# Kernel optimization log

Measured on AMD Instinct MI355X. Metric: run time of the kernel, lower is better.

## Reference

```python
import jax, jax.numpy as jnp
import numpy as np

S, B, E, D, A = 4096, 16, 1024, 1024, 512


def setup_inputs() -> dict:
    key = jax.random.key(0)
    ks = jax.random.split(key, 8)
    inv = lambda n: 1.0 / np.sqrt(n)
    return {
        "encoder_padded_last_layer_states": jax.random.normal(ks[0], (S, B, E), jnp.float32),
        "decoder_previous_time_step_state": jax.random.normal(ks[1], (1, B, D), jnp.float32),
        "We": jax.random.uniform(ks[2], (E, A), jnp.float32, -inv(E), inv(E)),
        "be": jax.random.uniform(ks[3], (A,), jnp.float32, -inv(E), inv(E)),
        "Wd": jax.random.uniform(ks[4], (D, A), jnp.float32, -inv(D), inv(D)),
        "bd": jax.random.uniform(ks[5], (A,), jnp.float32, -inv(D), inv(D)),
        "Ws": jax.random.uniform(ks[6], (A, 1), jnp.float32, -inv(A), inv(A)),
        "bs": jax.random.uniform(ks[7], (1,), jnp.float32, -inv(A), inv(A)),
    }


def reference(encoder_padded_last_layer_states, decoder_previous_time_step_state,
              We, be, Wd, bd, Ws, bs):
    enc = encoder_padded_last_layer_states  # [S, B, E]
    dec = decoder_previous_time_step_state  # [1, B, D]
    weighted_e = enc @ We + be              # [S, B, A]
    weighted_d = dec @ Wd + bd              # [1, B, A] broadcasts over S
    scores = jnp.tanh(weighted_e + weighted_d) @ Ws + bs  # [S, B, 1]
    alpha = jax.nn.softmax(scores, axis=0)  # softmax over time dim
    # alpha^T [B,1,S] bmm enc^T [B,S,E] -> [B,1,E] -> squeeze -> [B,E]
    contexts = jnp.einsum("sbo,sbe->be", alpha, enc)
    return contexts
```

## Files before the change

kernel.cpp:

```cpp
#include <hip/hip_runtime.h>
#include <hip/hip_bf16.h>

#define S_DIM 4096
#define B_DIM 16
#define E_DIM 1024
#define D_DIM 1024
#define A_DIM 512
#define M_DIM (S_DIM * B_DIM)
#define BK 64
#define NKS (E_DIM / BK)
#define MT 64

typedef __bf16 bf16x8 __attribute__((ext_vector_type(8)));
typedef float f32x4 __attribute__((ext_vector_type(4)));
typedef unsigned short u16;

__device__ __forceinline__ u16 f2bf(float f) {
    unsigned u = __builtin_bit_cast(unsigned, f);
    u += 0x7fffu + ((u >> 16) & 1u);
    return (u16)(u >> 16);
}
__device__ __forceinline__ unsigned pack2(float a, float b) {
    return (unsigned)f2bf(a) | ((unsigned)f2bf(b) << 16);
}

__device__ __forceinline__ void gload_lds16(const void* g, void* l) {
    __builtin_amdgcn_global_load_lds(
        (const __attribute__((address_space(1))) unsigned*)g,
        (__attribute__((address_space(3))) unsigned*)l, 16, 0, 0);
}

__global__ void k_prep_we(const float* __restrict__ We, u16* __restrict__ WeT) {
    const int gid = blockIdx.x * 256 + threadIdx.x;
    const int ks = gid >> 12, rem = gid & 4095;
    const int a = rem >> 3, d = rem & 7;
    const int c = d ^ (a & 7);
    const int e0 = ks * BK + c * 8;
    float v[8];
#pragma unroll
    for (int i = 0; i < 8; ++i) v[i] = We[(size_t)(e0 + i) * A_DIM + a];
    uint4 h;
    h.x = pack2(v[0], v[1]); h.y = pack2(v[2], v[3]);
    h.z = pack2(v[4], v[5]); h.w = pack2(v[6], v[7]);
    *reinterpret_cast<uint4*>(WeT + (size_t)ks * A_DIM * BK + a * BK + d * 8) = h;
}

__global__ void k_comb(const float* __restrict__ dec, const float* __restrict__ Wd,
                       const float* __restrict__ bd, const float* __restrict__ be,
                       float* __restrict__ comb) {
    __shared__ float red[4][64];
    const int a0 = blockIdx.x * 64;
    const int b = blockIdx.y;
    const int t = threadIdx.x;
    const int al = t & 63, w = t >> 6;
    float acc = 0.f;
    const float* dp = dec + (size_t)b * D_DIM + w * 256;
    const float* wp = Wd + (size_t)w * 256 * A_DIM + a0 + al;
    for (int d = 0; d < 256; ++d)
        acc += dp[d] * wp[(size_t)d * A_DIM];
    red[w][al] = acc;
    __syncthreads();
    if (t < 64)
        comb[b * A_DIM + a0 + t] =
            red[0][t] + red[1][t] + red[2][t] + red[3][t] + bd[a0 + t] + be[a0 + t];
}

__global__ __launch_bounds__(256, 2)
void k_scores(const float* __restrict__ enc, const u16* __restrict__ WeT,
              const float* __restrict__ comb, const float* __restrict__ Wsv,
              float* __restrict__ scores) {
    __shared__ __align__(16) u16 As[MT * BK];
    __shared__ __align__(16) u16 Bs[A_DIM * BK];

    const int tid = threadIdx.x;
    const int lane = tid & 63;
    const int wc = tid >> 6;
    const int l15 = lane & 15, lhi = lane >> 4;
    const int blockRow = blockIdx.x * MT;

    f32x4 acc[4][8];
#pragma unroll
    for (int mf = 0; mf < 4; ++mf)
#pragma unroll
        for (int nf = 0; nf < 8; ++nf)
            acc[mf][nf] = f32x4{0.f, 0.f, 0.f, 0.f};

    const int bOff = wc * 16384 + lane * 16;

    for (int ks = 0; ks < NKS; ++ks) {
        const int k0 = ks * BK;
        const char* gsrc = (const char*)WeT + (size_t)ks * A_DIM * BK * 2 + bOff;
        char* ldst = (char*)Bs + bOff;
#pragma unroll
        for (int i = 0; i < 16; ++i)
            gload_lds16(gsrc + i * 1024, ldst + i * 1024);
#pragma unroll
        for (int h = 0; h < 2; ++h) {
            const int g = tid + h * 256;
            const int r = g >> 3, d = g & 7;
            const int c = d ^ (r & 7);
            const float* src = enc + (size_t)(blockRow + r) * E_DIM + k0 + c * 8;
            const float4 v0 = *reinterpret_cast<const float4*>(src);
            const float4 v1 = *reinterpret_cast<const float4*>(src + 4);
            uint4 hh;
            hh.x = pack2(v0.x, v0.y); hh.y = pack2(v0.z, v0.w);
            hh.z = pack2(v1.x, v1.y); hh.w = pack2(v1.z, v1.w);
            *reinterpret_cast<uint4*>((char*)As + r * 128 + d * 16) = hh;
        }
        __syncthreads();
#pragma unroll
        for (int kk = 0; kk < 2; ++kk) {
            bf16x8 af[4];
#pragma unroll
            for (int mf = 0; mf < 4; ++mf) {
                const int rr = mf * 16 + l15;
                af[mf] = *reinterpret_cast<const bf16x8*>(
                    (const char*)As + rr * 128 + ((kk * 64 + lhi * 16) ^ ((rr & 7) << 4)));
            }
#pragma unroll
            for (int nf = 0; nf < 8; ++nf) {
                const int br = wc * 128 + nf * 16 + l15;
                const bf16x8 bfv = *reinterpret_cast<const bf16x8*>(
                    (const char*)Bs + br * 128 + ((kk * 64 + lhi * 16) ^ ((br & 7) << 4)));
#pragma unroll
                for (int mf = 0; mf < 4; ++mf)
                    acc[mf][nf] = __builtin_amdgcn_mfma_f32_16x16x32_bf16(
                        af[mf], bfv, acc[mf][nf], 0, 0, 0);
            }
        }
        __syncthreads();
    }

    float* combLDS = reinterpret_cast<float*>(Bs);
    float* sred = reinterpret_cast<float*>(As);
#pragma unroll
    for (int i = 0; i < 8; ++i) {
        const int idx = tid + i * 256;
        reinterpret_cast<float4*>(combLDS)[idx] = reinterpret_cast<const float4*>(comb)[idx];
    }
    if (tid < MT) sred[tid] = 0.f;
    __syncthreads();

    float part[4][4] = {};
#pragma unroll
    for (int nf = 0; nf < 8; ++nf) {
        const int C = wc * 128 + nf * 16 + l15;
        const float wsv = Wsv[C];
#pragma unroll
        for (int mf = 0; mf < 4; ++mf) {
#pragma unroll
            for (int j = 0; j < 4; ++j) {
                const int Rl = mf * 16 + lhi * 4 + j;
                const int b = (blockRow + Rl) & (B_DIM - 1);
                const float x = acc[mf][nf][j] + combLDS[b * A_DIM + C];
                const float e = __expf(-2.f * fabsf(x));
                float th = (1.f - e) / (1.f + e);
                th = (x < 0.f) ? -th : th;
                part[mf][j] += th * wsv;
            }
        }
    }
#pragma unroll
    for (int off = 1; off < 16; off <<= 1)
#pragma unroll
        for (int mf = 0; mf < 4; ++mf)
#pragma unroll
            for (int j = 0; j < 4; ++j)
                part[mf][j] += __shfl_xor(part[mf][j], off, 64);
    if (l15 == 0) {
#pragma unroll
        for (int mf = 0; mf < 4; ++mf)
#pragma unroll
            for (int j = 0; j < 4; ++j)
                atomicAdd(&sred[mf * 16 + lhi * 4 + j], part[mf][j]);
    }
    __syncthreads();
    if (tid < MT) {
        const int rr = blockRow + tid;
        scores[(size_t)(rr & (B_DIM - 1)) * S_DIM + (rr >> 4)] = sred[tid];
    }
}

__global__ void k_softmax(const float* __restrict__ scores, float* __restrict__ alpha) {
    __shared__ float red[8];
    const int b = blockIdx.x;
    const int tid = threadIdx.x;
    const float* sc = scores + (size_t)b * S_DIM;
    float m = -1e30f;
    for (int i = tid; i < S_DIM; i += 256) m = fmaxf(m, sc[i]);
#pragma unroll
    for (int off = 32; off; off >>= 1) m = fmaxf(m, __shfl_xor(m, off, 64));
    if ((tid & 63) == 0) red[tid >> 6] = m;
    __syncthreads();
    m = fmaxf(fmaxf(red[0], red[1]), fmaxf(red[2], red[3]));
    float s = 0.f;
    for (int i = tid; i < S_DIM; i += 256) s += __expf(sc[i] - m);
#pragma unroll
    for (int off = 32; off; off >>= 1) s += __shfl_xor(s, off, 64);
    if ((tid & 63) == 0) red[4 + (tid >> 6)] = s;
    __syncthreads();
    const float inv = 1.f / (red[4] + red[5] + red[6] + red[7]);
    float* al = alpha + (size_t)b * S_DIM;
    for (int i = tid; i < S_DIM; i += 256) al[i] = __expf(sc[i] - m) * inv;
}

__global__ void k_ctx1(const float* __restrict__ enc, const float* __restrict__ alpha,
                       float* __restrict__ partial) {
    const int b = blockIdx.y, ch = blockIdx.x, tid = threadIdx.x;
    const int s0 = ch * 64;
    float4 av = make_float4(0.f, 0.f, 0.f, 0.f);
    const float* al = alpha + (size_t)b * S_DIM + s0;
    for (int s = 0; s < 64; ++s) {
        const float a = al[s];
        const float4 v = *reinterpret_cast<const float4*>(
            enc + ((size_t)(s0 + s) * B_DIM + b) * E_DIM + tid * 4);
        av.x += a * v.x; av.y += a * v.y; av.z += a * v.z; av.w += a * v.w;
    }
    reinterpret_cast<float4*>(partial)[((size_t)b * 64 + ch) * 256 + tid] = av;
}

__global__ void k_ctx2(const float* __restrict__ partial, float* __restrict__ out) {
    const int b = blockIdx.x, tid = threadIdx.x;
    float4 s = make_float4(0.f, 0.f, 0.f, 0.f);
    for (int c = 0; c < 64; ++c) {
        const float4 v = reinterpret_cast<const float4*>(partial)[((size_t)b * 64 + c) * 256 + tid];
        s.x += v.x; s.y += v.y; s.z += v.z; s.w += v.w;
    }
    reinterpret_cast<float4*>(out)[b * 256 + tid] = s;
}

extern "C" void kernel_launch(void* const* d_in, const int* in_sizes, int n_in,
                              void* d_out, int out_size, void* d_ws, size_t ws_size,
                              hipStream_t stream) {
    const float* enc = (const float*)d_in[0];
    const float* dec = (const float*)d_in[1];
    const float* We  = (const float*)d_in[2];
    const float* be  = (const float*)d_in[3];
    const float* Wd  = (const float*)d_in[4];
    const float* bd  = (const float*)d_in[5];
    const float* Ws  = (const float*)d_in[6];
    float* out = (float*)d_out;

    char* ws = (char*)d_ws;
    u16*   WeT     = (u16*)ws;
    float* comb    = (float*)(ws + (1 << 20));
    float* scores  = (float*)(ws + (1 << 20) + (32 << 10));
    float* alpha   = (float*)(ws + (1 << 20) + (288 << 10));
    float* partial = (float*)(ws + (1 << 20) + (544 << 10));

    hipLaunchKernelGGL(k_prep_we, dim3(256), dim3(256), 0, stream, We, WeT);
    hipLaunchKernelGGL(k_comb, dim3(A_DIM / 64, B_DIM), dim3(256), 0, stream,
                       dec, Wd, bd, be, comb);
    hipLaunchKernelGGL(k_scores, dim3(M_DIM / MT), dim3(256), 0, stream,
                       enc, WeT, comb, Ws, scores);
    hipLaunchKernelGGL(k_softmax, dim3(B_DIM), dim3(256), 0, stream, scores, alpha);
    hipLaunchKernelGGL(k_ctx1, dim3(S_DIM / 64, B_DIM), dim3(256), 0, stream,
                       enc, alpha, partial);
    hipLaunchKernelGGL(k_ctx2, dim3(B_DIM), dim3(256), 0, stream, partial, out);
}
```

Measured before the change: 490.5 us.

## Restructure scores GEMM: 128-row tiles, register-prefetched A, direct global B loads

The scores kernel now uses 512 threads over 128-row tiles and double-buffers the bf16 encoder tile in LDS, prefetching the next k-slice into registers while MFMAs run. It drops the LDS staging of We and has each wave read B fragments straight from global memory, relying on the cache. WeT becomes a plain [A,E] bf16 layout built by an LDS-transposed prep kernel. Other changes: comb is read from global instead of LDS, bf16 conversion uses the native cast, the context split goes from 64 to 32 chunks, and some loops are unrolled. The risk is extra global and L2 traffic for the B operand, plus lower parallelism in the context stage.

```diff
diff --git a/kernel.cpp b/kernel.cpp
--- a/kernel.cpp
+++ b/kernel.cpp
@@ -9,40 +9,36 @@
 #define M_DIM (S_DIM * B_DIM)
 #define BK 64
 #define NKS (E_DIM / BK)
-#define MT 64
+#define MT 128
+#define CTX_CH 32
 
 typedef __bf16 bf16x8 __attribute__((ext_vector_type(8)));
+typedef __bf16 bf16x2 __attribute__((ext_vector_type(2)));
 typedef float f32x4 __attribute__((ext_vector_type(4)));
 typedef unsigned short u16;
 
-__device__ __forceinline__ u16 f2bf(float f) {
-    unsigned u = __builtin_bit_cast(unsigned, f);
-    u += 0x7fffu + ((u >> 16) & 1u);
-    return (u16)(u >> 16);
-}
 __device__ __forceinline__ unsigned pack2(float a, float b) {
-    return (unsigned)f2bf(a) | ((unsigned)f2bf(b) << 16);
-}
-
-__device__ __forceinline__ void gload_lds16(const void* g, void* l) {
-    __builtin_amdgcn_global_load_lds(
-        (const __attribute__((address_space(1))) unsigned*)g,
-        (__attribute__((address_space(3))) unsigned*)l, 16, 0, 0);
+    bf16x2 h;
+    h[0] = (__bf16)a;
+    h[1] = (__bf16)b;
+    return __builtin_bit_cast(unsigned, h);
 }
 
 __global__ void k_prep_we(const float* __restrict__ We, u16* __restrict__ WeT) {
-    const int gid = blockIdx.x * 256 + threadIdx.x;
-    const int ks = gid >> 12, rem = gid & 4095;
-    const int a = rem >> 3, d = rem & 7;
-    const int c = d ^ (a & 7);
-    const int e0 = ks * BK + c * 8;
-    float v[8];
-#pragma unroll
-    for (int i = 0; i < 8; ++i) v[i] = We[(size_t)(e0 + i) * A_DIM + a];
-    uint4 h;
-    h.x = pack2(v[0], v[1]); h.y = pack2(v[2], v[3]);
-    h.z = pack2(v[4], v[5]); h.w = pack2(v[6], v[7]);
-    *reinterpret_cast<uint4*>(WeT + (size_t)ks * A_DIM * BK + a * BK + d * 8) = h;
+    __shared__ float tile[32][33];
+    const int e0 = blockIdx.x * 32;
+    const int a0 = blockIdx.y * 32;
+    const int tx = threadIdx.x, ty = threadIdx.y;
+#pragma unroll
+    for (int i = 0; i < 32; i += 8)
+        tile[ty + i][tx] = We[(size_t)(e0 + ty + i) * A_DIM + a0 + tx];
+    __syncthreads();
+#pragma unroll
+    for (int i = 0; i < 32; i += 8) {
+        bf16x2 h; h[0] = (__bf16)tile[tx][ty + i]; h[1] = (__bf16)0.f;
+        WeT[(size_t)(a0 + ty + i) * E_DIM + e0 + tx] =
+            (u16)(__builtin_bit_cast(unsigned, h) & 0xffffu);
+    }
 }
 
 __global__ void k_comb(const float* __restrict__ dec, const float* __restrict__ Wd,
@@ -56,6 +52,7 @@
     float acc = 0.f;
     const float* dp = dec + (size_t)b * D_DIM + w * 256;
     const float* wp = Wd + (size_t)w * 256 * A_DIM + a0 + al;
+#pragma unroll 4
     for (int d = 0; d < 256; ++d)
         acc += dp[d] * wp[(size_t)d * A_DIM];
     red[w][al] = acc;
@@ -65,19 +62,23 @@
             red[0][t] + red[1][t] + red[2][t] + red[3][t] + bd[a0 + t] + be[a0 + t];
 }
 
-__global__ __launch_bounds__(256, 2)
+__global__ __launch_bounds__(512, 2)
 void k_scores(const float* __restrict__ enc, const u16* __restrict__ WeT,
               const float* __restrict__ comb, const float* __restrict__ Wsv,
               float* __restrict__ scores) {
-    __shared__ __align__(16) u16 As[MT * BK];
-    __shared__ __align__(16) u16 Bs[A_DIM * BK];
+    __shared__ __align__(16) u16 As[2][MT * BK];
+    __shared__ float sred[MT];
 
     const int tid = threadIdx.x;
     const int lane = tid & 63;
-    const int wc = tid >> 6;
+    const int wave = tid >> 6;
+    const int wr = wave >> 2;
+    const int wc = wave & 3;
     const int l15 = lane & 15, lhi = lane >> 4;
     const int blockRow = blockIdx.x * MT;
 
+    if (tid < MT) sred[tid] = 0.f;
+
     f32x4 acc[4][8];
 #pragma unroll
     for (int mf = 0; mf < 4; ++mf)
@@ -85,74 +86,94 @@
         for (int nf = 0; nf < 8; ++nf)
             acc[mf][nf] = f32x4{0.f, 0.f, 0.f, 0.f};
 
-    const int bOff = wc * 16384 + lane * 16;
+    const int sr0 = tid >> 3, sd = tid & 7;
+
+    float4 pv[4];
+#pragma unroll
+    for (int h = 0; h < 2; ++h) {
+        const int r = sr0 + h * 64;
+        const int c = sd ^ (r & 7);
+        const float* src = enc + (size_t)(blockRow + r) * E_DIM + c * 8;
+        pv[2 * h]     = *reinterpret_cast<const float4*>(src);
+        pv[2 * h + 1] = *reinterpret_cast<const float4*>(src + 4);
+    }
+#pragma unroll
+    for (int h = 0; h < 2; ++h) {
+        const int r = sr0 + h * 64;
+        uint4 hh;
+        hh.x = pack2(pv[2 * h].x, pv[2 * h].y);
+        hh.y = pack2(pv[2 * h].z, pv[2 * h].w);
+        hh.z = pack2(pv[2 * h + 1].x, pv[2 * h + 1].y);
+        hh.w = pack2(pv[2 * h + 1].z, pv[2 * h + 1].w);
+        *reinterpret_cast<uint4*>((char*)As[0] + r * 128 + sd * 16) = hh;
+    }
+    __syncthreads();
+
+    const u16* bbase = WeT + (size_t)(wc * 128 + l15) * E_DIM + lhi * 8;
 
     for (int ks = 0; ks < NKS; ++ks) {
+        const int cb = ks & 1;
         const int k0 = ks * BK;
-        const char* gsrc = (const char*)WeT + (size_t)ks * A_DIM * BK * 2 + bOff;
-        char* ldst = (char*)Bs + bOff;
-#pragma unroll
-        for (int i = 0; i < 16; ++i)
-            gload_lds16(gsrc + i * 1024, ldst + i * 1024);
-#pragma unroll
-        for (int h = 0; h < 2; ++h) {
-            const int g = tid + h * 256;
-            const int r = g >> 3, d = g & 7;
-            const int c = d ^ (r & 7);
-            const float* src = enc + (size_t)(blockRow + r) * E_DIM + k0 + c * 8;
-            const float4 v0 = *reinterpret_cast<const float4*>(src);
-            const float4 v1 = *reinterpret_cast<const float4*>(src + 4);
-            uint4 hh;
-            hh.x = pack2(v0.x, v0.y); hh.y = pack2(v0.z, v0.w);
-            hh.z = pack2(v1.x, v1.y); hh.w = pack2(v1.z, v1.w);
-            *reinterpret_cast<uint4*>((char*)As + r * 128 + d * 16) = hh;
-        }
-        __syncthreads();
+        if (ks + 1 < NKS) {
+#pragma unroll
+            for (int h = 0; h < 2; ++h) {
+                const int r = sr0 + h * 64;
+                const int c = sd ^ (r & 7);
+                const float* src = enc + (size_t)(blockRow + r) * E_DIM + (k0 + BK) + c * 8;
+                pv[2 * h]     = *reinterpret_cast<const float4*>(src);
+                pv[2 * h + 1] = *reinterpret_cast<const float4*>(src + 4);
+            }
+        }
 #pragma unroll
         for (int kk = 0; kk < 2; ++kk) {
             bf16x8 af[4];
 #pragma unroll
             for (int mf = 0; mf < 4; ++mf) {
-                const int rr = mf * 16 + l15;
+                const int rr = wr * 64 + mf * 16 + l15;
                 af[mf] = *reinterpret_cast<const bf16x8*>(
-                    (const char*)As + rr * 128 + ((kk * 64 + lhi * 16) ^ ((rr & 7) << 4)));
-            }
-#pragma unroll
-            for (int nf = 0; nf < 8; ++nf) {
-                const int br = wc * 128 + nf * 16 + l15;
-                const bf16x8 bfv = *reinterpret_cast<const bf16x8*>(
-                    (const char*)Bs + br * 128 + ((kk * 64 + lhi * 16) ^ ((br & 7) << 4)));
+                    (const char*)As[cb] + rr * 128 + ((kk * 64 + lhi * 16) ^ ((rr & 7) << 4)));
+            }
+            bf16x8 bq[8];
+#pragma unroll
+            for (int nf = 0; nf < 8; ++nf)
+                bq[nf] = *reinterpret_cast<const bf16x8*>(
+                    bbase + (size_t)nf * 16 * E_DIM + k0 + kk * 32);
+#pragma unroll
+            for (int nf = 0; nf < 8; ++nf)
 #pragma unroll
                 for (int mf = 0; mf < 4; ++mf)
                     acc[mf][nf] = __builtin_amdgcn_mfma_f32_16x16x32_bf16(
-                        af[mf], bfv, acc[mf][nf], 0, 0, 0);
+                        af[mf], bq[nf], acc[mf][nf], 0, 0, 0);
+        }
+        if (ks + 1 < NKS) {
+#pragma unroll
+            for (int h = 0; h < 2; ++h) {
+                const int r = sr0 + h * 64;
+                uint4 hh;
+                hh.x = pack2(pv[2 * h].x, pv[2 * h].y);
+                hh.y = pack2(pv[2 * h].z, pv[2 * h].w);
+                hh.z = pack2(pv[2 * h + 1].x, pv[2 * h + 1].y);
+                hh.w = pack2(pv[2 * h + 1].z, pv[2 * h + 1].w);
+                *reinterpret_cast<uint4*>((char*)As[cb ^ 1] + r * 128 + sd * 16) = hh;
             }
         }
         __syncthreads();
     }
-
-    float* combLDS = reinterpret_cast<float*>(Bs);
-    float* sred = reinterpret_cast<float*>(As);
-#pragma unroll
-    for (int i = 0; i < 8; ++i) {
-        const int idx = tid + i * 256;
-        reinterpret_cast<float4*>(combLDS)[idx] = reinterpret_cast<const float4*>(comb)[idx];
-    }
-    if (tid < MT) sred[tid] = 0.f;
-    __syncthreads();
 
     float part[4][4] = {};
 #pragma unroll
     for (int nf = 0; nf < 8; ++nf) {
         const int C = wc * 128 + nf * 16 + l15;
         const float wsv = Wsv[C];
+        float cbv[4];
+#pragma unroll
+        for (int j = 0; j < 4; ++j)
+            cbv[j] = comb[(lhi * 4 + j) * A_DIM + C];
 #pragma unroll
         for (int mf = 0; mf < 4; ++mf) {
 #pragma unroll
             for (int j = 0; j < 4; ++j) {
-                const int Rl = mf * 16 + lhi * 4 + j;
-                const int b = (blockRow + Rl) & (B_DIM - 1);
-                const float x = acc[mf][nf][j] + combLDS[b * A_DIM + C];
+                const float x = acc[mf][nf][j] + cbv[j];
                 const float e = __expf(-2.f * fabsf(x));
                 float th = (1.f - e) / (1.f + e);
                 th = (x < 0.f) ? -th : th;
@@ -172,7 +193,7 @@
         for (int mf = 0; mf < 4; ++mf)
 #pragma unroll
             for (int j = 0; j < 4; ++j)
-                atomicAdd(&sred[mf * 16 + lhi * 4 + j], part[mf][j]);
+                atomicAdd(&sred[wr * 64 + mf * 16 + lhi * 4 + j], part[mf][j]);
     }
     __syncthreads();
     if (tid < MT) {
@@ -207,23 +228,26 @@
 __global__ void k_ctx1(const float* __restrict__ enc, const float* __restrict__ alpha,
                        float* __restrict__ partial) {
     const int b = blockIdx.y, ch = blockIdx.x, tid = threadIdx.x;
-    const int s0 = ch * 64;
+    const int s0 = ch * (S_DIM / CTX_CH);
     float4 av = make_float4(0.f, 0.f, 0.f, 0.f);
     const float* al = alpha + (size_t)b * S_DIM + s0;
-    for (int s = 0; s < 64; ++s) {
+#pragma unroll 4
+    for (int s = 0; s < S_DIM / CTX_CH; ++s) {
         const float a = al[s];
         const float4 v = *reinterpret_cast<const float4*>(
             enc + ((size_t)(s0 + s) * B_DIM + b) * E_DIM + tid * 4);
         av.x += a * v.x; av.y += a * v.y; av.z += a * v.z; av.w += a * v.w;
     }
-    reinterpret_cast<float4*>(partial)[((size_t)b * 64 + ch) * 256 + tid] = av;
+    reinterpret_cast<float4*>(partial)[((size_t)b * CTX_CH + ch) * 256 + tid] = av;
 }
 
 __global__ void k_ctx2(const float* __restrict__ partial, float* __restrict__ out) {
     const int b = blockIdx.x, tid = threadIdx.x;
     float4 s = make_float4(0.f, 0.f, 0.f, 0.f);
-    for (int c = 0; c < 64; ++c) {
-        const float4 v = reinterpret_cast<const float4*>(partial)[((size_t)b * 64 + c) * 256 + tid];
+#pragma unroll
+    for (int c = 0; c < CTX_CH; ++c) {
+        const float4 v =
+            reinterpret_cast<const float4*>(partial)[((size_t)b * CTX_CH + c) * 256 + tid];
         s.x += v.x; s.y += v.y; s.z += v.z; s.w += v.w;
     }
     reinterpret_cast<float4*>(out)[b * 256 + tid] = s;
@@ -248,13 +272,14 @@
     float* alpha   = (float*)(ws + (1 << 20) + (288 << 10));
     float* partial = (float*)(ws + (1 << 20) + (544 << 10));
 
-    hipLaunchKernelGGL(k_prep_we, dim3(256), dim3(256), 0, stream, We, WeT);
+    hipLaunchKernelGGL(k_prep_we, dim3(E_DIM / 32, A_DIM / 32), dim3(32, 8), 0, stream,
+                       We, WeT);
     hipLaunchKernelGGL(k_comb, dim3(A_DIM / 64, B_DIM), dim3(256), 0, stream,
                        dec, Wd, bd, be, comb);
-    hipLaunchKernelGGL(k_scores, dim3(M_DIM / MT), dim3(256), 0, stream,
+    hipLaunchKernelGGL(k_scores, dim3(M_DIM / MT), dim3(512), 0, stream,
                        enc, WeT, comb, Ws, scores);
     hipLaunchKernelGGL(k_softmax, dim3(B_DIM), dim3(256), 0, stream, scores, alpha);
-    hipLaunchKernelGGL(k_ctx1, dim3(S_DIM / 64, B_DIM), dim3(256), 0, stream,
+    hipLaunchKernelGGL(k_ctx1, dim3(CTX_CH, B_DIM), dim3(256), 0, stream,
                        enc, alpha, partial);
     hipLaunchKernelGGL(k_ctx2, dim3(B_DIM), dim3(256), 0, stream, partial, out);
 }
```

Result: slower. 580.5 us (+18.4%).
